# Kernel optimization log

Measured on AMD Instinct MI355X. Metric: run time of the kernel, lower is better.

The kernel has to match this reference:

```python
import jax, jax.numpy as jnp
import numpy as np

B, A = 4096, 8          # episodes, agents per episode
N = B * A               # total nodes
E = B * A * (A - 1)     # fully-connected directed edges within each group
F_IN, D, H, M, NA = 64, 64, 4, 64, 10  # in_feat, gnn_dim, heads, mem_dim, n_actions
NEG_SLOPE = 0.2
LN_EPS = 1e-5


def _build_edge_index():
    base = np.arange(A)
    s = np.repeat(base, A)
    d = np.tile(base, A)
    keep = s != d
    s, d = s[keep], d[keep]                       # [A*(A-1)]
    offs = (np.arange(B) * A)[:, None]
    src = (offs + s[None, :]).reshape(-1)
    dst = (offs + d[None, :]).reshape(-1)
    return jnp.asarray(np.stack([src, dst]), dtype=jnp.int32)  # [2, E]


def setup_inputs() -> dict:
    key = jax.random.key(0)
    ks = jax.random.split(key, 16)
    sc = 0.05
    return {
        "x": jax.random.normal(ks[0], (N, F_IN), jnp.float32),
        "edge_attr": jax.random.normal(ks[1], (E, 3), jnp.float32),
        "hidden": jax.random.normal(ks[2], (N, M), jnp.float32) * sc,
        "edge_index": _build_edge_index(),
        # GATv2 params
        "Wl": jax.random.normal(ks[3], (H * D, F_IN), jnp.float32) * sc,
        "bl": jnp.zeros((H * D,), jnp.float32),
        "Wr": jax.random.normal(ks[4], (H * D, F_IN), jnp.float32) * sc,
        "br": jnp.zeros((H * D,), jnp.float32),
        "We": jax.random.normal(ks[5], (H * D, 3), jnp.float32) * sc,
        "be": jnp.zeros((H * D,), jnp.float32),
        "att": jax.random.normal(ks[6], (H, D), jnp.float32) * sc,
        "bias_g": jnp.zeros((D,), jnp.float32),
        # GRUCell params (gate order r,z,n as in torch)
        "W_ih": jax.random.normal(ks[7], (3 * M, D), jnp.float32) * sc,
        "W_hh": jax.random.normal(ks[8], (3 * M, M), jnp.float32) * sc,
        "b_ih": jnp.zeros((3 * M,), jnp.float32),
        "b_hh": jnp.zeros((3 * M,), jnp.float32),
        # LayerNorm + output Linear
        "ln_g": jnp.ones((M,), jnp.float32),
        "ln_b": jnp.zeros((M,), jnp.float32),
        "Wq": jax.random.normal(ks[9], (NA, M), jnp.float32) * sc,
        "bq": jnp.zeros((NA,), jnp.float32),
    }


def reference(x, edge_attr, hidden, edge_index, Wl, bl, Wr, br, We, be, att,
              bias_g, W_ih, W_hh, b_ih, b_hh, ln_g, ln_b, Wq, bq):
    src, dst = edge_index[0], edge_index[1]
    # GATv2Conv (concat=False -> mean over heads), share_weights=False
    xl = (x @ Wl.T + bl).reshape(N, H, D)          # source projection
    xr = (x @ Wr.T + br).reshape(N, H, D)          # target projection
    ee = (edge_attr @ We.T + be).reshape(E, H, D)  # edge embedding
    m = jax.nn.leaky_relu(xl[src] + xr[dst] + ee, NEG_SLOPE)  # [E,H,D]
    logits = jnp.einsum('ehd,hd->eh', m, att)                  # [E,H]
    lmax = jax.ops.segment_max(logits, dst, num_segments=N)    # [N,H]
    ex = jnp.exp(logits - lmax[dst])
    denom = jax.ops.segment_sum(ex, dst, num_segments=N)       # [N,H]
    alpha = ex / denom[dst]                                    # softmax per target
    agg = jax.ops.segment_sum(alpha[:, :, None] * xl[src], dst, num_segments=N)  # [N,H,D]
    h_gnn = jax.nn.relu(agg.mean(axis=1) + bias_g)             # [N,D]
    # GRUCell
    gi = h_gnn @ W_ih.T + b_ih
    gh = hidden @ W_hh.T + b_hh
    ir, iz, inn = jnp.split(gi, 3, axis=-1)
    hr, hz, hn = jnp.split(gh, 3, axis=-1)
    r = jax.nn.sigmoid(ir + hr)
    z = jax.nn.sigmoid(iz + hz)
    n = jnp.tanh(inn + r * hn)
    h = (1.0 - z) * n + z * hidden                              # [N,M]
    # LayerNorm + Linear head
    mu = h.mean(axis=-1, keepdims=True)
    var = ((h - mu) ** 2).mean(axis=-1, keepdims=True)
    hln = (h - mu) / jnp.sqrt(var + LN_EPS) * ln_g + ln_b
    q = hln @ Wq.T + bq                                         # [N,NA]
    return q, h
```

## Files before the change

### kernel.cpp

```cpp
#include <hip/hip_runtime.h>

typedef unsigned short u16;
typedef __attribute__((ext_vector_type(8))) short bf16x8;
typedef __attribute__((ext_vector_type(4))) float f32x4;
typedef _Float16 f16;
typedef __attribute__((ext_vector_type(2))) f16 h2;
typedef __attribute__((ext_vector_type(8))) f16 h8;

#define NAG 8
#define NAGB 16
#define FIN 64
#define MDIM 64
#define NACT 10
#define EPG 56
#define NTOT 32768
#define ABP 72
#define XLS 296
#define XHS 72

#define U_XR  4736
#define U_RZ  0
#define U_HN  2048
#define U_LN  3072
#define U_INB 8320

__device__ __forceinline__ float b2f(u16 u) {
  return __uint_as_float(((unsigned int)u) << 16);
}
__device__ __forceinline__ u16 f2b(float f) {
  unsigned int x = __float_as_uint(f);
  unsigned int r = x + 0x7fffu + ((x >> 16) & 1u);
  return (u16)(r >> 16);
}
__device__ __forceinline__ u16 f2h(float f) {
  f16 h = (f16)f; u16 u; __builtin_memcpy(&u, &h, 2); return u;
}
__device__ __forceinline__ float h2f(u16 u) {
  f16 h; __builtin_memcpy(&h, &u, 2); return (float)h;
}

union H8u { h8 v; h2 p[4]; };

__device__ __forceinline__ h8 lrelu8(h8 m) {
  h8 s = m * (f16)0.2f;
#if __has_builtin(__builtin_elementwise_max)
  return __builtin_elementwise_max(m, s);
#else
  h8 r;
#pragma unroll
  for (int i = 0; i < 8; i++) r[i] = (m[i] > s[i]) ? m[i] : s[i];
  return r;
#endif
}

__device__ __forceinline__ float dotacc(h2 a, h2 b, float c) {
  c += (float)a[0] * (float)b[0];
  c += (float)a[1] * (float)b[1];
  return c;
}

__global__ __launch_bounds__(256) void prep_weights(
    const float* __restrict__ Wl, const float* __restrict__ Wr,
    const float* __restrict__ Wih, const float* __restrict__ Whh,
    u16* __restrict__ wsB)
{
  const int idx = blockIdx.x * 256 + threadIdx.x;
  if (idx >= 56 * 2 * 64) return;
  const int L  = idx & 63;
  const int ks = (idx >> 6) & 1;
  const int T  = idx >> 7;
  const float* W; int row0;
  if      (T < 16) { W = Wl;  row0 = T * 16; }
  else if (T < 32) { W = Wr;  row0 = (T - 16) * 16; }
  else if (T < 44) { W = Wih; row0 = (T - 32) * 16; }
  else             { W = Whh; row0 = (T - 44) * 16; }
  const int row = row0 + (L & 15);
  const int k0  = ks * 32 + (L >> 4) * 8;
  u16 v[8];
#pragma unroll
  for (int j = 0; j < 8; j++) v[j] = f2b(W[row * 64 + k0 + j]);
  *(bf16x8*)(wsB + (size_t)idx * 8) = *(bf16x8*)v;
}

__global__ __launch_bounds__(256, 4) void gnn_rnn_kernel(
    const float* __restrict__ x, const float* __restrict__ edge_attr,
    const float* __restrict__ hidden,
    const float* __restrict__ bl, const float* __restrict__ br,
    const float* __restrict__ We, const float* __restrict__ be,
    const float* __restrict__ att, const float* __restrict__ bias_g,
    const float* __restrict__ b_ih, const float* __restrict__ b_hh,
    const float* __restrict__ ln_g, const float* __restrict__ ln_b,
    const float* __restrict__ Wq, const float* __restrict__ bq,
    const u16* __restrict__ wsB,
    float* __restrict__ d_out)
{
  __shared__ __align__(16) char uraw[18944];
  __shared__ __align__(16) u16 s_xb[NAGB * ABP];
  __shared__ __align__(16) u16 s_hidb[NAGB * ABP];
  __shared__ __align__(16) u16 s_hgb[NAGB * ABP];
  __shared__ float s_ea[2 * EPG * 3];
  __shared__ __align__(16) u16 s_blh[256], s_brh[256];
  __shared__ __align__(16) u16 s_w0h[256], s_w1h[256], s_w2h[256], s_atth[256];
  __shared__ float s_alpha[2 * EPG][4];

  u16*   uXL  = (u16*)uraw;
  u16*   uXR  = (u16*)uraw + U_XR;
  u16*   uInn = (u16*)uraw + U_INB;
  float* uF   = (float*)uraw;

  const int t = threadIdx.x;
  const int b = blockIdx.x;
  const int L = t & 63;
  const int w = t >> 6;
  const int q = L >> 4;

  {
    const float* xb = x + b * (NAGB * FIN);
    const float* hb = hidden + b * (NAGB * MDIM);
#pragma unroll
    for (int i = t; i < NAGB * FIN; i += 256) {
      const int a = i >> 6, m = i & 63;
      s_xb[a * ABP + m] = f2b(xb[i]);
      s_hidb[a * ABP + m] = f2b(hb[i]);
    }
    const float* eb = edge_attr + b * (2 * EPG * 3);
    for (int i = t; i < 2 * EPG * 3; i += 256) s_ea[i] = eb[i];
    s_blh[t]  = f2h(bl[t]);
    s_brh[t]  = f2h(br[t] + be[t]);
    s_w0h[t]  = f2h(We[t * 3]);
    s_w1h[t]  = f2h(We[t * 3 + 1]);
    s_w2h[t]  = f2h(We[t * 3 + 2]);
    s_atth[t] = f2h(att[t]);
  }
  __syncthreads();

  {
    const int arow = L & 15;
    bf16x8 af0 = *(const bf16x8*)&s_xb[arow * ABP + q * 8];
    bf16x8 af1 = *(const bf16x8*)&s_xb[arow * ABP + 32 + q * 8];
    const bf16x8* wsBv = (const bf16x8*)wsB;
#pragma unroll 4
    for (int i = 0; i < 8; i++) {
      const int T = w * 8 + i;
      f32x4 acc = {0.f, 0.f, 0.f, 0.f};
      acc = __builtin_amdgcn_mfma_f32_16x16x32_bf16(af0, wsBv[(T * 2 + 0) * 64 + L], acc, 0, 0, 0);
      acc = __builtin_amdgcn_mfma_f32_16x16x32_bf16(af1, wsBv[(T * 2 + 1) * 64 + L], acc, 0, 0, 0);
      const int col = L & 15;
      const int Tm = T & 15;
      const int h = Tm >> 2, d = (Tm & 3) * 16 + col;
      const int gc = Tm * 16 + col;
      if (T < 16) {
        const float bias = h2f(s_blh[gc]);
#pragma unroll
        for (int r = 0; r < 4; r++)
          uXL[(q * 4 + r) * XLS + h * XHS + d] = f2h(acc[r] + bias);
      } else {
        const float bias = h2f(s_brh[gc]);
#pragma unroll
        for (int r = 0; r < 4; r++)
          uXR[(q * 4 + r) * XLS + h * XHS + d] = f2h(acc[r] + bias);
      }
    }
  }
  __syncthreads();

  {
    const int h = w;
    if (L < EPG) {
      const int e = L;
      const int s = e / 7, k = e % 7;
      const int j = k + (k >= s ? 1 : 0);
      const float* ea0 = s_ea + e * 3;
      const float* ea1 = s_ea + (EPG + e) * 3;
      const f16 a00 = (f16)ea0[0], a01 = (f16)ea0[1], a02 = (f16)ea0[2];
      const f16 a10 = (f16)ea1[0], a11 = (f16)ea1[1], a12 = (f16)ea1[2];
      const u16* xlp0 = uXL + s * XLS + h * XHS;
      const u16* xrp0 = uXR + j * XLS + h * XHS;
      const u16* xlp1 = uXL + (8 + s) * XLS + h * XHS;
      const u16* xrp1 = uXR + (8 + j) * XLS + h * XHS;
      const u16* w0p = s_w0h + h * 64;
      const u16* w1p = s_w1h + h * 64;
      const u16* w2p = s_w2h + h * 64;
      const u16* atp = s_atth + h * 64;
      float lgA0 = 0.f, lgB0 = 0.f, lgA1 = 0.f, lgB1 = 0.f;
#pragma unroll 2
      for (int kq = 0; kq < 8; kq++) {
        H8u w0, w1, w2, at, x0, r0, x1, r1, m0, m1;
        w0.v = *(const h8*)(w0p + kq * 8);
        w1.v = *(const h8*)(w1p + kq * 8);
        w2.v = *(const h8*)(w2p + kq * 8);
        at.v = *(const h8*)(atp + kq * 8);
        x0.v = *(const h8*)(xlp0 + kq * 8);
        r0.v = *(const h8*)(xrp0 + kq * 8);
        x1.v = *(const h8*)(xlp1 + kq * 8);
        r1.v = *(const h8*)(xrp1 + kq * 8);
        m0.v = x0.v + r0.v + w0.v * a00 + w1.v * a01 + w2.v * a02;
        m0.v = lrelu8(m0.v);
        m1.v = x1.v + r1.v + w0.v * a10 + w1.v * a11 + w2.v * a12;
        m1.v = lrelu8(m1.v);
        lgA0 = dotacc(m0.p[0], at.p[0], lgA0);
        lgB0 = dotacc(m0.p[1], at.p[1], lgB0);
        lgA0 = dotacc(m0.p[2], at.p[2], lgA0);
        lgB0 = dotacc(m0.p[3], at.p[3], lgB0);
        lgA1 = dotacc(m1.p[0], at.p[0], lgA1);
        lgB1 = dotacc(m1.p[1], at.p[1], lgB1);
        lgA1 = dotacc(m1.p[2], at.p[2], lgA1);
        lgB1 = dotacc(m1.p[3], at.p[3], lgB1);
      }
      s_alpha[e][h]       = lgA0 + lgB0;
      s_alpha[EPG + e][h] = lgA1 + lgB1;
    }
  }
  __syncthreads();

  if (t < 64) {
    const int ep = t >> 5, j = (t >> 2) & 7, h = t & 3;
    const int e0 = ep * EPG;
    float mx = -1e30f;
#pragma unroll
    for (int s = 0; s < 8; s++) {
      if (s == j) continue;
      int e = e0 + s * 7 + (j > s ? j - 1 : j);
      mx = fmaxf(mx, s_alpha[e][h]);
    }
    float sum = 0.f;
#pragma unroll
    for (int s = 0; s < 8; s++) {
      if (s == j) continue;
      int e = e0 + s * 7 + (j > s ? j - 1 : j);
      float ex = __expf(s_alpha[e][h] - mx);
      s_alpha[e][h] = ex;
      sum += ex;
    }
    float inv = 1.f / sum;
#pragma unroll
    for (int s = 0; s < 8; s++) {
      if (s == j) continue;
      int e = e0 + s * 7 + (j > s ? j - 1 : j);
      s_alpha[e][h] *= inv;
    }
  }
  __syncthreads();

  {
    const int ep = t >> 7, jj = (t >> 4) & 7, dq = t & 15;
    const int a16 = ep * 8 + jj;
    float acc[4] = {0.f, 0.f, 0.f, 0.f};
#pragma unroll 2
    for (int h = 0; h < 4; h++) {
#pragma unroll
      for (int s = 0; s < 8; s++) {
        if (s == jj) continue;
        int e = ep * EPG + s * 7 + (jj > s ? jj - 1 : jj);
        float al = s_alpha[e][h];
        const u16* xp = uXL + (ep * 8 + s) * XLS + h * XHS + dq * 4;
        ushort4 xv = *(const ushort4*)xp;
        acc[0] += al * h2f(xv.x);
        acc[1] += al * h2f(xv.y);
        acc[2] += al * h2f(xv.z);
        acc[3] += al * h2f(xv.w);
      }
    }
    const f32x4 bg = *(const f32x4*)(bias_g + dq * 4);
    u16 pk[4];
#pragma unroll
    for (int c = 0; c < 4; c++) {
      float v = acc[c] * 0.25f + bg[c];
      pk[c] = f2b(v > 0.f ? v : 0.f);
    }
    *(uint2*)&s_hgb[a16 * ABP + dq * 4] = *(uint2*)pk;
  }
  __syncthreads();

  {
    const int arow = L & 15;
    bf16x8 ag0 = *(const bf16x8*)&s_hgb[arow * ABP + q * 8];
    bf16x8 ag1 = *(const bf16x8*)&s_hgb[arow * ABP + 32 + q * 8];
    bf16x8 ah0 = *(const bf16x8*)&s_hidb[arow * ABP + q * 8];
    bf16x8 ah1 = *(const bf16x8*)&s_hidb[arow * ABP + 32 + q * 8];
    const bf16x8* wsBv = (const bf16x8*)wsB;
#pragma unroll
    for (int i = 0; i < 3; i++) {
      const int T6 = w * 3 + i;
      const int Tg = 32 + T6, Th = 44 + T6;
      f32x4 acci = {0.f, 0.f, 0.f, 0.f};
      acci = __builtin_amdgcn_mfma_f32_16x16x32_bf16(ag0, wsBv[(Tg * 2 + 0) * 64 + L], acci, 0, 0, 0);
      acci = __builtin_amdgcn_mfma_f32_16x16x32_bf16(ag1, wsBv[(Tg * 2 + 1) * 64 + L], acci, 0, 0, 0);
      f32x4 acch = {0.f, 0.f, 0.f, 0.f};
      acch = __builtin_amdgcn_mfma_f32_16x16x32_bf16(ah0, wsBv[(Th * 2 + 0) * 64 + L], acch, 0, 0, 0);
      acch = __builtin_amdgcn_mfma_f32_16x16x32_bf16(ah1, wsBv[(Th * 2 + 1) * 64 + L], acch, 0, 0, 0);
      const int col = L & 15;
      const int gc = T6 * 16 + col;
      if (T6 < 8) {
        const float bsum = b_ih[gc] + b_hh[gc];
#pragma unroll
        for (int r = 0; r < 4; r++)
          uF[U_RZ + (q * 4 + r) * 128 + gc] = acci[r] + acch[r] + bsum;
      } else {
        const float bi = b_ih[gc], bh = b_hh[gc];
#pragma unroll
        for (int r = 0; r < 4; r++) {
          uInn[(q * 4 + r) * 64 + gc - 128] = f2b(acci[r] + bi);
          uF[U_HN + (q * 4 + r) * 64 + gc - 128] = acch[r] + bh;
        }
      }
    }
  }
  __syncthreads();

  {
    const float lng = ln_g[L];
    const float lnb = ln_b[L];
#pragma unroll
    for (int rr = 0; rr < 4; rr++) {
      const int a = w + rr * 4, m = L;
      float rz_r = uF[U_RZ + a * 128 + m];
      float rz_z = uF[U_RZ + a * 128 + 64 + m];
      float inn  = b2f(uInn[a * 64 + m]);
      float hn   = uF[U_HN + a * 64 + m];
      float hid  = b2f(s_hidb[a * ABP + m]);
      float r = 1.f / (1.f + __expf(-rz_r));
      float z = 1.f / (1.f + __expf(-rz_z));
      float xg = inn + r * hn;
      xg = fminf(fmaxf(xg, -20.f), 20.f);
      float e2 = __expf(2.f * xg);
      float n = (e2 - 1.f) / (e2 + 1.f);
      float hv = (1.f - z) * n + z * hid;
      d_out[NTOT * NACT + (b * NAGB + a) * MDIM + m] = hv;
      float sum = hv;
#pragma unroll
      for (int off = 1; off < 64; off <<= 1) sum += __shfl_xor(sum, off, 64);
      float mu = sum * (1.f / 64.f);
      float dv = hv - mu;
      float s2 = dv * dv;
#pragma unroll
      for (int off = 1; off < 64; off <<= 1) s2 += __shfl_xor(s2, off, 64);
      float var = s2 * (1.f / 64.f);
      uF[U_LN + a * 68 + m] = dv * rsqrtf(var + 1e-5f) * lng + lnb;
    }
  }
  __syncthreads();

  if (t < NAGB * NACT) {
    const int a = t / NACT, o = t % NACT;
    float acc = bq[o];
    const float4* lv = (const float4*)(uF + U_LN + a * 68);
    const float4* wv = (const float4*)(Wq + o * 64);
#pragma unroll 4
    for (int kq = 0; kq < 16; kq++) {
      float4 l4 = lv[kq], w4 = wv[kq];
      acc += l4.x * w4.x + l4.y * w4.y + l4.z * w4.z + l4.w * w4.w;
    }
    d_out[(b * NAGB + a) * NACT + o] = acc;
  }
}

extern "C" void kernel_launch(void* const* d_in, const int* in_sizes, int n_in,
                              void* d_out, int out_size, void* d_ws, size_t ws_size,
                              hipStream_t stream) {
  const int N  = in_sizes[0] / FIN;
  const int Bn = N / NAGB;
  u16* wsB = (u16*)d_ws;

  prep_weights<<<28, 256, 0, stream>>>(
      (const float*)d_in[4],
      (const float*)d_in[6],
      (const float*)d_in[12],
      (const float*)d_in[13],
      wsB);

  gnn_rnn_kernel<<<Bn, 256, 0, stream>>>(
      (const float*)d_in[0], (const float*)d_in[1], (const float*)d_in[2],
      (const float*)d_in[5],
      (const float*)d_in[7],
      (const float*)d_in[8],
      (const float*)d_in[9],
      (const float*)d_in[10],
      (const float*)d_in[11],
      (const float*)d_in[14],
      (const float*)d_in[15],
      (const float*)d_in[16], (const float*)d_in[17],
      (const float*)d_in[18], (const float*)d_in[19],
      wsB, (float*)d_out);
}
```

Baseline: 145.2 us.

## Shrink LDS footprint via aliasing and raise occupancy target to six blocks

```diff
diff --git a/kernel.cpp b/kernel.cpp
--- a/kernel.cpp
+++ b/kernel.cpp
@@ -22,6 +22,7 @@
 #define U_RZ  0
 #define U_HN  2048
 #define U_LN  3072
+#define U_HG  6144
 #define U_INB 8320
 
 __device__ __forceinline__ float b2f(u16 u) {
@@ -82,7 +83,7 @@
   *(bf16x8*)(wsB + (size_t)idx * 8) = *(bf16x8*)v;
 }
 
-__global__ __launch_bounds__(256, 4) void gnn_rnn_kernel(
+__global__ __launch_bounds__(256, 6) void gnn_rnn_kernel(
     const float* __restrict__ x, const float* __restrict__ edge_attr,
     const float* __restrict__ hidden,
     const float* __restrict__ bl, const float* __restrict__ br,
@@ -95,18 +96,17 @@
     float* __restrict__ d_out)
 {
   __shared__ __align__(16) char uraw[18944];
-  __shared__ __align__(16) u16 s_xb[NAGB * ABP];
+  __shared__ __align__(16) u16 u2raw[NAGB * ABP];
   __shared__ __align__(16) u16 s_hidb[NAGB * ABP];
-  __shared__ __align__(16) u16 s_hgb[NAGB * ABP];
-  __shared__ float s_ea[2 * EPG * 3];
-  __shared__ __align__(16) u16 s_blh[256], s_brh[256];
   __shared__ __align__(16) u16 s_w0h[256], s_w1h[256], s_w2h[256], s_atth[256];
-  __shared__ float s_alpha[2 * EPG][4];
 
   u16*   uXL  = (u16*)uraw;
   u16*   uXR  = (u16*)uraw + U_XR;
   u16*   uInn = (u16*)uraw + U_INB;
+  u16*   s_hgb = (u16*)uraw + U_HG;
   float* uF   = (float*)uraw;
+  u16*   s_xb = u2raw;
+  float (*s_alpha)[4] = (float(*)[4])u2raw;
 
   const int t = threadIdx.x;
   const int b = blockIdx.x;
@@ -123,14 +123,16 @@
       s_xb[a * ABP + m] = f2b(xb[i]);
       s_hidb[a * ABP + m] = f2b(hb[i]);
     }
-    const float* eb = edge_attr + b * (2 * EPG * 3);
-    for (int i = t; i < 2 * EPG * 3; i += 256) s_ea[i] = eb[i];
-    s_blh[t]  = f2h(bl[t]);
-    s_brh[t]  = f2h(br[t] + be[t]);
     s_w0h[t]  = f2h(We[t * 3]);
     s_w1h[t]  = f2h(We[t * 3 + 1]);
     s_w2h[t]  = f2h(We[t * 3 + 2]);
     s_atth[t] = f2h(att[t]);
+  }
+  float ea00 = 0.f, ea01 = 0.f, ea02 = 0.f, ea10 = 0.f, ea11 = 0.f, ea12 = 0.f;
+  if (L < EPG) {
+    const float* eb = edge_attr + b * (2 * EPG * 3) + L * 3;
+    ea00 = eb[0]; ea01 = eb[1]; ea02 = eb[2];
+    ea10 = eb[EPG * 3]; ea11 = eb[EPG * 3 + 1]; ea12 = eb[EPG * 3 + 2];
   }
   __syncthreads();
 
@@ -150,12 +152,12 @@
       const int h = Tm >> 2, d = (Tm & 3) * 16 + col;
       const int gc = Tm * 16 + col;
       if (T < 16) {
-        const float bias = h2f(s_blh[gc]);
+        const float bias = bl[gc];
 #pragma unroll
         for (int r = 0; r < 4; r++)
           uXL[(q * 4 + r) * XLS + h * XHS + d] = f2h(acc[r] + bias);
       } else {
-        const float bias = h2f(s_brh[gc]);
+        const float bias = br[gc] + be[gc];
 #pragma unroll
         for (int r = 0; r < 4; r++)
           uXR[(q * 4 + r) * XLS + h * XHS + d] = f2h(acc[r] + bias);
@@ -170,10 +172,8 @@
       const int e = L;
       const int s = e / 7, k = e % 7;
       const int j = k + (k >= s ? 1 : 0);
-      const float* ea0 = s_ea + e * 3;
-      const float* ea1 = s_ea + (EPG + e) * 3;
-      const f16 a00 = (f16)ea0[0], a01 = (f16)ea0[1], a02 = (f16)ea0[2];
-      const f16 a10 = (f16)ea1[0], a11 = (f16)ea1[1], a12 = (f16)ea1[2];
+      const f16 a00 = (f16)ea00, a01 = (f16)ea01, a02 = (f16)ea02;
+      const f16 a10 = (f16)ea10, a11 = (f16)ea11, a12 = (f16)ea12;
       const u16* xlp0 = uXL + s * XLS + h * XHS;
       const u16* xrp0 = uXR + j * XLS + h * XHS;
       const u16* xlp1 = uXL + (8 + s) * XLS + h * XHS;
@@ -213,8 +213,10 @@
   }
   __syncthreads();
 
-  if (t < 64) {
-    const int ep = t >> 5, j = (t >> 2) & 7, h = t & 3;
+  if (L < 16) {
+    const int ep = w & 1;
+    const int j = ((w >> 1) << 2) + (L >> 2);
+    const int h = L & 3;
     const int e0 = ep * EPG;
     float mx = -1e30f;
 #pragma unroll
@@ -327,16 +329,16 @@
       float n = (e2 - 1.f) / (e2 + 1.f);
       float hv = (1.f - z) * n + z * hid;
       d_out[NTOT * NACT + (b * NAGB + a) * MDIM + m] = hv;
-      float sum = hv;
-#pragma unroll
-      for (int off = 1; off < 64; off <<= 1) sum += __shfl_xor(sum, off, 64);
-      float mu = sum * (1.f / 64.f);
-      float dv = hv - mu;
-      float s2 = dv * dv;
-#pragma unroll
-      for (int off = 1; off < 64; off <<= 1) s2 += __shfl_xor(s2, off, 64);
-      float var = s2 * (1.f / 64.f);
-      uF[U_LN + a * 68 + m] = dv * rsqrtf(var + 1e-5f) * lng + lnb;
+      float sum = hv, sq = hv * hv;
+#pragma unroll
+      for (int off = 1; off < 64; off <<= 1) {
+        sum += __shfl_xor(sum, off, 64);
+        sq  += __shfl_xor(sq,  off, 64);
+      }
+      float mu  = sum * (1.f / 64.f);
+      float var = sq * (1.f / 64.f) - mu * mu;
+      var = var > 0.f ? var : 0.f;
+      uF[U_LN + a * 68 + m] = (hv - mu) * rsqrtf(var + 1e-5f) * lng + lnb;
     }
   }
   __syncthreads();
```

New measurement: 145.3 us. About the same (+0.0%).
